# Optimization experiments

Measured on AMD Instinct MI355X. Metric: run time of the kernel, lower is better.

## Reference

```python
import jax, jax.numpy as jnp
import numpy as np

N, E, C, FIN, FOUT = 4096, 5, 2, 128, 64
DENSITY = 0.01


def setup_inputs() -> dict:
    key = jax.random.key(0)
    ks = jax.random.split(key, 8)
    vals = jax.random.uniform(ks[0], (E, N, N), dtype=jnp.float32)
    mask = jax.random.uniform(ks[1], (E, N, N)) < DENSITY
    A = jnp.where(mask, vals, 0.0)                      # [E,N,N] edge-type adjacencies (A[e,u,v]: u->v)
    h = jax.random.normal(ks[2], (N, FIN), dtype=jnp.float32)
    W1_0 = 0.01 * jax.random.normal(ks[3], (C, E), dtype=jnp.float32)  # GTConv init: normal(std=0.01)
    W2_0 = 0.01 * jax.random.normal(ks[4], (C, E), dtype=jnp.float32)
    W1_1 = 0.01 * jax.random.normal(ks[5], (C, E), dtype=jnp.float32)
    gcn_W = jax.random.normal(ks[6], (C, FIN, FOUT), dtype=jnp.float32) / np.sqrt(FIN)
    gcn_b = jnp.zeros((C, FOUT), dtype=jnp.float32)
    return {"A": A, "h": h, "W1_0": W1_0, "W2_0": W2_0, "W1_1": W1_1,
            "gcn_W": gcn_W, "gcn_b": gcn_b}


def reference(A, h, W1_0, W2_0, W1_1, gcn_W, gcn_b):
    # Structural support of the summed graphs (union of edge-type edges).
    mask = (A != 0).any(axis=0)                         # [N,N]

    def gtconv(filt):
        # weighted sum of edge-type adjacencies per channel: dgl.adj_sum_graph
        return jnp.einsum('ce,euv->cuv', filt, A)       # [C,N,N]

    def right_norm(M, sum_axis):
        # EdgeWeightNorm(norm='right'): divide each edge weight by total in-weight at dst
        d = M.sum(axis=sum_axis, keepdims=True)
        return M / jnp.where(d != 0, d, 1.0)

    def softmax_norm(S):
        # exp on existing edges only, then right-normalize over in-edges (src axis=1)
        w = jnp.where(mask, jnp.exp(S), 0.0)
        return right_norm(w, sum_axis=1)

    # Layer 0 (first=True)
    RA = softmax_norm(gtconv(W1_0))                     # first_adj, [C,N,N]
    RB = softmax_norm(gtconv(W2_0))
    H0 = jnp.einsum('cuk,ckv->cuv', RA, RB)             # dgl.adj_product_graph
    # Layer 1 (first=False): result_A = H0, result_B = conv1(A) (no softmax)
    RB1 = gtconv(W1_1)
    H1 = jnp.einsum('cuk,ckv->cuv', H0, RB1)

    layers = jnp.stack([RA, H0, H1], axis=1)            # [C,3,N,N] = layer_list per channel
    Wn = right_norm(layers, sum_axis=2)                 # right norm over src (axis u)
    # GraphConv(norm='none', activation=relu) with edge_weight: out[v] = relu(sum_u w[u,v] h[u] W + b)
    agg = jnp.einsum('cluv,uf->clvf', Wn, h)            # [C,3,N,FIN]
    out = jax.nn.relu(jnp.einsum('clvf,cfo->clvo', agg, gcn_W) + gcn_b[:, None, None, :])
    return out                                          # [C,3,N,FOUT]
```

## Files before the change

### kernel.cpp

```cpp
#include <hip/hip_runtime.h>
#include <hip/hip_bf16.h>

#define NN    4096
#define NE    5
#define NC    2
#define FINF  128
#define FOUTF 64
#define CAP   384


static __device__ __forceinline__ unsigned bf16bits(float x)
{
    __hip_bfloat16 t = __float2bfloat16(x);
    return (unsigned)*reinterpret_cast<unsigned short*>(&t);
}

__global__ __launch_bounds__(256) void init_misc(int4* __restrict__ cnt4,
                                                 const float4* __restrict__ h4,
                                                 uint2* __restrict__ hb)
{
    int b = blockIdx.x;
    if (b < 4) {
        cnt4[b * 256 + threadIdx.x] = int4{0, 0, 0, 0};
    } else {
        int i = (b - 4) * 256 + threadIdx.x;
        float4 f = h4[i];
        uint2 r;
        r.x = bf16bits(f.x) | (bf16bits(f.y) << 16);
        r.y = bf16bits(f.z) | (bf16bits(f.w) << 16);
        hb[i] = r;
    }
}

__global__ __launch_bounds__(256) void build_csc(
    const float* __restrict__ A,
    const float* __restrict__ W1_0,
    const float* __restrict__ W2_0,
    const float* __restrict__ W1_1,
    int*    __restrict__ cnt,
    int*    __restrict__ eu,
    float2* __restrict__ wA,
    float2* __restrict__ wB,
    float2* __restrict__ wC)
{
    float fA0[NE], fA1[NE], fB0[NE], fB1[NE], fC0[NE], fC1[NE];
#pragma unroll
    for (int e = 0; e < NE; ++e) {
        fA0[e] = W1_0[e];      fA1[e] = W1_0[NE + e];
        fB0[e] = W2_0[e];      fB1[e] = W2_0[NE + e];
        fC0[e] = W1_1[e];      fC1[e] = W1_1[NE + e];
    }

    const size_t S = (size_t)NN * NN / 4;
    const float4* A4 = (const float4*)A;
    size_t stride = (size_t)gridDim.x * blockDim.x;
    for (size_t i = (size_t)blockIdx.x * blockDim.x + threadIdx.x; i < S; i += stride) {
        float4 q0 = A4[i];
        float4 q1 = A4[i + S];
        float4 q2 = A4[i + 2 * S];
        float4 q3 = A4[i + 3 * S];
        float4 q4 = A4[i + 4 * S];
        int u  = (int)(i >> 10);
        int v0 = ((int)i & 1023) << 2;
#define DO_COMP(comp, joff)                                                      \
        {                                                                        \
            float a0 = q0.comp, a1 = q1.comp, a2 = q2.comp,                      \
                  a3 = q3.comp, a4 = q4.comp;                                    \
            if (a0 != 0.f || a1 != 0.f || a2 != 0.f || a3 != 0.f || a4 != 0.f) { \
                float sA0 = fA0[0]*a0 + fA0[1]*a1 + fA0[2]*a2 + fA0[3]*a3 + fA0[4]*a4; \
                float sA1 = fA1[0]*a0 + fA1[1]*a1 + fA1[2]*a2 + fA1[3]*a3 + fA1[4]*a4; \
                float sB0 = fB0[0]*a0 + fB0[1]*a1 + fB0[2]*a2 + fB0[3]*a3 + fB0[4]*a4; \
                float sB1 = fB1[0]*a0 + fB1[1]*a1 + fB1[2]*a2 + fB1[3]*a3 + fB1[4]*a4; \
                float sC0 = fC0[0]*a0 + fC0[1]*a1 + fC0[2]*a2 + fC0[3]*a3 + fC0[4]*a4; \
                float sC1 = fC1[0]*a0 + fC1[1]*a1 + fC1[2]*a2 + fC1[3]*a3 + fC1[4]*a4; \
                int v = v0 + joff;                                               \
                int pos = atomicAdd(&cnt[v], 1);                                 \
                if (pos < CAP) {                                                 \
                    int slot = v * CAP + pos;                                    \
                    eu[slot] = u;                                                \
                    wA[slot] = float2{__expf(sA0), __expf(sA1)};                 \
                    wB[slot] = float2{__expf(sB0), __expf(sB1)};                 \
                    wC[slot] = float2{sC0, sC1};                                 \
                }                                                                \
            }                                                                    \
        }
        DO_COMP(x, 0)
        DO_COMP(y, 1)
        DO_COMP(z, 2)
        DO_COMP(w, 3)
#undef DO_COMP
    }
}

template<int STAGE>
__global__ __launch_bounds__(256) void spmm_col(
    const int*    __restrict__ cnt,
    const int*    __restrict__ eu,
    const float2* __restrict__ ew,
    const uint2*  __restrict__ Xb_in,
    const float*  __restrict__ Dd_in,
    const float*  __restrict__ gW,
    const float*  __restrict__ gb,
    float*        __restrict__ out,
    ushort*       __restrict__ Xb_out,
    float*        __restrict__ Dd_out)
{
    int v = blockIdx.x;
    int n = cnt[v];
    if (n > CAP) n = CAP;

    __shared__ float4 s_e[CAP];
    __shared__ float  s_red[4];
    __shared__ float4 s_acc[NC][8][32];
    __shared__ float  s_y[NC][FINF];
    __shared__ float  s_inv[NC];

    int tid = threadIdx.x;
    if (tid < 4) s_red[tid] = 0.f;
    __syncthreads();

    float l0 = 0.f, l1 = 0.f, ld0 = 0.f, ld1 = 0.f;
    for (int i = tid; i < n; i += 256) {
        int    u = eu[v * CAP + i];
        float2 w = ew[v * CAP + i];
        s_e[i] = float4{__int_as_float(u), w.x, w.y, 0.f};
        l0 += w.x;
        l1 += w.y;
        if (STAGE != 0) {
            ld0 += w.x * Dd_in[u];
            ld1 += w.y * Dd_in[NN + u];
        }
    }
    if (STAGE == 0) { ld0 = l0; ld1 = l1; }

#pragma unroll
    for (int m = 32; m >= 1; m >>= 1) {
        l0  += __shfl_xor(l0,  m);
        l1  += __shfl_xor(l1,  m);
        ld0 += __shfl_xor(ld0, m);
        ld1 += __shfl_xor(ld1, m);
    }
    if ((tid & 63) == 0) {
        atomicAdd(&s_red[0], l0);
        atomicAdd(&s_red[1], l1);
        atomicAdd(&s_red[2], ld0);
        atomicAdd(&s_red[3], ld1);
    }
    __syncthreads();

    int grp = tid >> 5, lane = tid & 31;
    float4 a0 = {0.f, 0.f, 0.f, 0.f};
    float4 a1 = {0.f, 0.f, 0.f, 0.f};

    if (STAGE == 0) {
#pragma unroll 2
        for (int i = grp; i < n; i += 8) {
            float4 e = s_e[i];
            uint2 b = Xb_in[(size_t)__float_as_int(e.x) * 32 + lane];
            float x0 = __uint_as_float(b.x << 16);
            float x1 = __uint_as_float(b.x & 0xffff0000u);
            float x2 = __uint_as_float(b.y << 16);
            float x3 = __uint_as_float(b.y & 0xffff0000u);
            a0.x += e.y * x0; a0.y += e.y * x1; a0.z += e.y * x2; a0.w += e.y * x3;
            a1.x += e.z * x0; a1.y += e.z * x1; a1.z += e.z * x2; a1.w += e.z * x3;
        }
    } else {
        const uint2* P0 = Xb_in;
        const uint2* P1 = Xb_in + (size_t)NN * 32;
#pragma unroll 2
        for (int i = grp; i < n; i += 8) {
            float4 e = s_e[i];
            int u = __float_as_int(e.x);
            uint2 b0 = P0[(size_t)u * 32 + lane];
            uint2 b1 = P1[(size_t)u * 32 + lane];
            a0.x += e.y * __uint_as_float(b0.x << 16);
            a0.y += e.y * __uint_as_float(b0.x & 0xffff0000u);
            a0.z += e.y * __uint_as_float(b0.y << 16);
            a0.w += e.y * __uint_as_float(b0.y & 0xffff0000u);
            a1.x += e.z * __uint_as_float(b1.x << 16);
            a1.y += e.z * __uint_as_float(b1.x & 0xffff0000u);
            a1.z += e.z * __uint_as_float(b1.y << 16);
            a1.w += e.z * __uint_as_float(b1.y & 0xffff0000u);
        }
    }

    s_acc[0][grp][lane] = a0;
    s_acc[1][grp][lane] = a1;
    __syncthreads();

    int c = tid >> 7, f = tid & 127;
    {
        const float* base = (const float*)s_acc[c];
        float s = 0.f;
#pragma unroll
        for (int g = 0; g < 8; ++g) s += base[g * 128 + f];

        float inv = 1.f;
        if (STAGE < 2 && n > 0) inv = 1.f / s_red[c];
        float val = s * inv;

        s_y[c][f] = val;
        if (STAGE < 2)
            Xb_out[((size_t)c * NN + v) * FINF + f] = (ushort)bf16bits(val);
        if (f == 0) {
            float dvn = s_red[2 + c] * inv;
            s_inv[c] = (dvn != 0.f) ? (1.f / dvn) : 1.f;
            if (STAGE < 2) Dd_out[c * NN + v] = dvn;
        }
    }
    __syncthreads();

    if (tid < 2 * FOUTF) {
        int c2 = tid >> 6, o = tid & 63;
        const float* w = gW + (size_t)c2 * FINF * FOUTF + o;
        const float* y = s_y[c2];
        float acc = 0.f;
#pragma unroll 8
        for (int f2 = 0; f2 < FINF; ++f2)
            acc += y[f2] * w[(size_t)f2 * FOUTF];
        float r = acc * s_inv[c2] + gb[c2 * FOUTF + o];
        out[(((size_t)c2 * 3 + STAGE) * NN + v) * FOUTF + o] = fmaxf(r, 0.f);
    }
}

extern "C" void kernel_launch(void* const* d_in, const int* in_sizes, int n_in,
                              void* d_out, int out_size, void* d_ws, size_t ws_size,
                              hipStream_t stream)
{
    const float* A     = (const float*)d_in[0];
    const float* h     = (const float*)d_in[1];
    const float* W1_0  = (const float*)d_in[2];
    const float* W2_0  = (const float*)d_in[3];
    const float* W1_1  = (const float*)d_in[4];
    const float* gW    = (const float*)d_in[5];
    const float* gb    = (const float*)d_in[6];
    float* out = (float*)d_out;

    char* ws = (char*)d_ws;
    int*    cnt = (int*)(ws);
    int*    eu  = (int*)(ws + 16384);
    float2* wA  = (float2*)(ws + 6307840);
    float2* wB  = (float2*)(ws + 18890752);
    float2* wC  = (float2*)(ws + 31473664);
    float*  DdA = (float*)(ws + 44056576);
    float*  Dd1 = (float*)(ws + 44089344);
    uint2*  hb  = (uint2*)(ws + 44122112);
    ushort* XbA = (ushort*)(ws + 45170688);
    ushort* Xb1 = (ushort*)(ws + 47267840);

    init_misc<<<516, 256, 0, stream>>>((int4*)cnt, (const float4*)h, hb);
    build_csc<<<2048, 256, 0, stream>>>(A, W1_0, W2_0, W1_1, cnt, eu, wA, wB, wC);

    spmm_col<0><<<NN, 256, 0, stream>>>(cnt, eu, wA, hb, nullptr, gW, gb, out, XbA, DdA);
    spmm_col<1><<<NN, 256, 0, stream>>>(cnt, eu, wB, (const uint2*)XbA, DdA, gW, gb, out, Xb1, Dd1);
    spmm_col<2><<<NN, 256, 0, stream>>>(cnt, eu, wC, (const uint2*)Xb1, Dd1, gW, gb, out, nullptr, nullptr);
}
```

Measured before the change: 224.5 us.

## Pack edge records into one int4 with fp16 weights; switch features to fp16

Replaces the separate index and three float2 weight arrays with a single 16-byte record per edge that holds the source index and fp16-packed weight pairs for all three stages. The build kernel now writes one vector store per edge instead of four scattered stores, and each SpMM stage reads one record. Intermediate feature matrices switch from bf16 to fp16, which keeps the same storage size but gives more mantissa bits. The cost is extra fp16 conversion work, and exp-valued or unnormalized weights risk overflow or precision loss in half precision.

```diff
diff --git a/kernel.cpp b/kernel.cpp
--- a/kernel.cpp
+++ b/kernel.cpp
@@ -1,5 +1,4 @@
 #include <hip/hip_runtime.h>
-#include <hip/hip_bf16.h>
 
 #define NN    4096
 #define NE    5
@@ -9,15 +8,28 @@
 #define CAP   384
 
 
-static __device__ __forceinline__ unsigned bf16bits(float x)
-{
-    __hip_bfloat16 t = __float2bfloat16(x);
-    return (unsigned)*reinterpret_cast<unsigned short*>(&t);
+union f16u { unsigned short s; _Float16 h; };
+
+static __device__ __forceinline__ unsigned short f2h(float x)
+{
+    f16u u; u.h = (_Float16)x; return u.s;
+}
+static __device__ __forceinline__ float lo16f(unsigned x)
+{
+    f16u u; u.s = (unsigned short)(x & 0xffff); return (float)u.h;
+}
+static __device__ __forceinline__ float hi16f(unsigned x)
+{
+    f16u u; u.s = (unsigned short)(x >> 16); return (float)u.h;
+}
+static __device__ __forceinline__ unsigned pack2h(float a, float b)
+{
+    return (unsigned)f2h(a) | ((unsigned)f2h(b) << 16);
 }
 
 __global__ __launch_bounds__(256) void init_misc(int4* __restrict__ cnt4,
                                                  const float4* __restrict__ h4,
-                                                 uint2* __restrict__ hb)
+                                                 uint2* __restrict__ hh)
 {
     int b = blockIdx.x;
     if (b < 4) {
@@ -26,9 +38,9 @@
         int i = (b - 4) * 256 + threadIdx.x;
         float4 f = h4[i];
         uint2 r;
-        r.x = bf16bits(f.x) | (bf16bits(f.y) << 16);
-        r.y = bf16bits(f.z) | (bf16bits(f.w) << 16);
-        hb[i] = r;
+        r.x = pack2h(f.x, f.y);
+        r.y = pack2h(f.z, f.w);
+        hh[i] = r;
     }
 }
 
@@ -37,11 +49,8 @@
     const float* __restrict__ W1_0,
     const float* __restrict__ W2_0,
     const float* __restrict__ W1_1,
-    int*    __restrict__ cnt,
-    int*    __restrict__ eu,
-    float2* __restrict__ wA,
-    float2* __restrict__ wB,
-    float2* __restrict__ wC)
+    int*  __restrict__ cnt,
+    int4* __restrict__ epack)
 {
     float fA0[NE], fA1[NE], fB0[NE], fB1[NE], fC0[NE], fC1[NE];
 #pragma unroll
@@ -76,11 +85,12 @@
                 int v = v0 + joff;                                               \
                 int pos = atomicAdd(&cnt[v], 1);                                 \
                 if (pos < CAP) {                                                 \
-                    int slot = v * CAP + pos;                                    \
-                    eu[slot] = u;                                                \
-                    wA[slot] = float2{__expf(sA0), __expf(sA1)};                 \
-                    wB[slot] = float2{__expf(sB0), __expf(sB1)};                 \
-                    wC[slot] = float2{sC0, sC1};                                 \
+                    int4 rec;                                                    \
+                    rec.x = u;                                                   \
+                    rec.y = (int)pack2h(__expf(sA0), __expf(sA1));               \
+                    rec.z = (int)pack2h(__expf(sB0), __expf(sB1));               \
+                    rec.w = (int)pack2h(sC0, sC1);                               \
+                    epack[v * CAP + pos] = rec;                                  \
                 }                                                                \
             }                                                                    \
         }
@@ -94,16 +104,15 @@
 
 template<int STAGE>
 __global__ __launch_bounds__(256) void spmm_col(
-    const int*    __restrict__ cnt,
-    const int*    __restrict__ eu,
-    const float2* __restrict__ ew,
-    const uint2*  __restrict__ Xb_in,
-    const float*  __restrict__ Dd_in,
-    const float*  __restrict__ gW,
-    const float*  __restrict__ gb,
-    float*        __restrict__ out,
-    ushort*       __restrict__ Xb_out,
-    float*        __restrict__ Dd_out)
+    const int*   __restrict__ cnt,
+    const int4*  __restrict__ epack,
+    const uint2* __restrict__ Xh_in,
+    const float* __restrict__ Dd_in,
+    const float* __restrict__ gW,
+    const float* __restrict__ gb,
+    float*       __restrict__ out,
+    unsigned short* __restrict__ Xh_out,
+    float*       __restrict__ Dd_out)
 {
     int v = blockIdx.x;
     int n = cnt[v];
@@ -121,14 +130,15 @@
 
     float l0 = 0.f, l1 = 0.f, ld0 = 0.f, ld1 = 0.f;
     for (int i = tid; i < n; i += 256) {
-        int    u = eu[v * CAP + i];
-        float2 w = ew[v * CAP + i];
-        s_e[i] = float4{__int_as_float(u), w.x, w.y, 0.f};
-        l0 += w.x;
-        l1 += w.y;
+        int4 E = epack[v * CAP + i];
+        unsigned wb = (unsigned)((STAGE == 0) ? E.y : (STAGE == 1) ? E.z : E.w);
+        float w0 = lo16f(wb), w1 = hi16f(wb);
+        s_e[i] = float4{__int_as_float(E.x), w0, w1, 0.f};
+        l0 += w0;
+        l1 += w1;
         if (STAGE != 0) {
-            ld0 += w.x * Dd_in[u];
-            ld1 += w.y * Dd_in[NN + u];
+            ld0 += w0 * Dd_in[E.x];
+            ld1 += w1 * Dd_in[NN + E.x];
         }
     }
     if (STAGE == 0) { ld0 = l0; ld1 = l1; }
@@ -156,31 +166,25 @@
 #pragma unroll 2
         for (int i = grp; i < n; i += 8) {
             float4 e = s_e[i];
-            uint2 b = Xb_in[(size_t)__float_as_int(e.x) * 32 + lane];
-            float x0 = __uint_as_float(b.x << 16);
-            float x1 = __uint_as_float(b.x & 0xffff0000u);
-            float x2 = __uint_as_float(b.y << 16);
-            float x3 = __uint_as_float(b.y & 0xffff0000u);
+            uint2 b = Xh_in[(size_t)__float_as_int(e.x) * 32 + lane];
+            float x0 = lo16f(b.x), x1 = hi16f(b.x);
+            float x2 = lo16f(b.y), x3 = hi16f(b.y);
             a0.x += e.y * x0; a0.y += e.y * x1; a0.z += e.y * x2; a0.w += e.y * x3;
             a1.x += e.z * x0; a1.y += e.z * x1; a1.z += e.z * x2; a1.w += e.z * x3;
         }
     } else {
-        const uint2* P0 = Xb_in;
-        const uint2* P1 = Xb_in + (size_t)NN * 32;
+        const uint2* P0 = Xh_in;
+        const uint2* P1 = Xh_in + (size_t)NN * 32;
 #pragma unroll 2
         for (int i = grp; i < n; i += 8) {
             float4 e = s_e[i];
             int u = __float_as_int(e.x);
             uint2 b0 = P0[(size_t)u * 32 + lane];
             uint2 b1 = P1[(size_t)u * 32 + lane];
-            a0.x += e.y * __uint_as_float(b0.x << 16);
-            a0.y += e.y * __uint_as_float(b0.x & 0xffff0000u);
-            a0.z += e.y * __uint_as_float(b0.y << 16);
-            a0.w += e.y * __uint_as_float(b0.y & 0xffff0000u);
-            a1.x += e.z * __uint_as_float(b1.x << 16);
-            a1.y += e.z * __uint_as_float(b1.x & 0xffff0000u);
-            a1.z += e.z * __uint_as_float(b1.y << 16);
-            a1.w += e.z * __uint_as_float(b1.y & 0xffff0000u);
+            a0.x += e.y * lo16f(b0.x); a0.y += e.y * hi16f(b0.x);
+            a0.z += e.y * lo16f(b0.y); a0.w += e.y * hi16f(b0.y);
+            a1.x += e.z * lo16f(b1.x); a1.y += e.z * hi16f(b1.x);
+            a1.z += e.z * lo16f(b1.y); a1.w += e.z * hi16f(b1.y);
         }
     }
 
@@ -201,7 +205,7 @@
 
         s_y[c][f] = val;
         if (STAGE < 2)
-            Xb_out[((size_t)c * NN + v) * FINF + f] = (ushort)bf16bits(val);
+            Xh_out[((size_t)c * NN + v) * FINF + f] = f2h(val);
         if (f == 0) {
             float dvn = s_red[2 + c] * inv;
             s_inv[c] = (dvn != 0.f) ? (1.f / dvn) : 1.f;
@@ -237,21 +241,18 @@
     float* out = (float*)d_out;
 
     char* ws = (char*)d_ws;
-    int*    cnt = (int*)(ws);
-    int*    eu  = (int*)(ws + 16384);
-    float2* wA  = (float2*)(ws + 6307840);
-    float2* wB  = (float2*)(ws + 18890752);
-    float2* wC  = (float2*)(ws + 31473664);
-    float*  DdA = (float*)(ws + 44056576);
-    float*  Dd1 = (float*)(ws + 44089344);
-    uint2*  hb  = (uint2*)(ws + 44122112);
-    ushort* XbA = (ushort*)(ws + 45170688);
-    ushort* Xb1 = (ushort*)(ws + 47267840);
-
-    init_misc<<<516, 256, 0, stream>>>((int4*)cnt, (const float4*)h, hb);
-    build_csc<<<2048, 256, 0, stream>>>(A, W1_0, W2_0, W1_1, cnt, eu, wA, wB, wC);
-
-    spmm_col<0><<<NN, 256, 0, stream>>>(cnt, eu, wA, hb, nullptr, gW, gb, out, XbA, DdA);
-    spmm_col<1><<<NN, 256, 0, stream>>>(cnt, eu, wB, (const uint2*)XbA, DdA, gW, gb, out, Xb1, Dd1);
-    spmm_col<2><<<NN, 256, 0, stream>>>(cnt, eu, wC, (const uint2*)Xb1, Dd1, gW, gb, out, nullptr, nullptr);
-}
+    int*            cnt   = (int*)(ws);
+    int4*           epack = (int4*)(ws + 16384);
+    float*          DdA   = (float*)(ws + 25182208);
+    float*          Dd1   = (float*)(ws + 25214976);
+    uint2*          hh    = (uint2*)(ws + 25247744);
+    unsigned short* XhA   = (unsigned short*)(ws + 26296320);
+    unsigned short* Xh1   = (unsigned short*)(ws + 28393472);
+
+    init_misc<<<516, 256, 0, stream>>>((int4*)cnt, (const float4*)h, hh);
+    build_csc<<<2048, 256, 0, stream>>>(A, W1_0, W2_0, W1_1, cnt, epack);
+
+    spmm_col<0><<<NN, 256, 0, stream>>>(cnt, epack, hh, nullptr, gW, gb, out, XhA, DdA);
+    spmm_col<1><<<NN, 256, 0, stream>>>(cnt, epack, (const uint2*)XhA, DdA, gW, gb, out, Xh1, Dd1);
+    spmm_col<2><<<NN, 256, 0, stream>>>(cnt, epack, (const uint2*)Xh1, Dd1, gW, gb, out, nullptr, nullptr);
+}
```

New measurement: 212.1 us. 1.06x faster.
